# Kernel tuning notes

Hardware: AMD Instinct MI355X
Metric: run time of the kernel (lower is better)

## Reference

```python
import jax, jax.numpy as jnp
import numpy as np

N, IN_DIM = 50000, 1024
E = 100000
NUM_REL = 40
HEADS, OUT_DIM = 4, 200
HID = HEADS * OUT_DIM  # 800
B = 8192
NEG_SLOPE = 0.2


def setup_inputs() -> dict:
    key = jax.random.key(0)
    ks = jax.random.split(key, 12)
    node_emb = jax.random.normal(ks[0], (N, IN_DIM), dtype=jnp.float32)
    # RelGAT learnable params
    W = jax.random.normal(ks[1], (IN_DIM, HID), dtype=jnp.float32) * (1.0 / np.sqrt(IN_DIM))
    bias = jnp.zeros((HID,), dtype=jnp.float32)
    a_src = jax.random.normal(ks[2], (HEADS, OUT_DIM), dtype=jnp.float32) * 0.1
    a_dst = jax.random.normal(ks[3], (HEADS, OUT_DIM), dtype=jnp.float32) * 0.1
    a_rel = jax.random.normal(ks[4], (HEADS, OUT_DIM), dtype=jnp.float32) * 0.1
    rel_feat = jax.random.normal(ks[5], (NUM_REL, HID), dtype=jnp.float32) * 0.1
    # DistMult scorer relation embeddings
    rel_emb = jax.random.normal(ks[6], (NUM_REL, HID), dtype=jnp.float32) * 0.1
    # Graph structure (constants)
    edge_index = jax.random.randint(ks[7], (2, E), 0, N, dtype=jnp.int64)
    edge_type = jax.random.randint(ks[8], (E,), 0, NUM_REL, dtype=jnp.int64)
    # Triple batch
    src_ids = jax.random.randint(ks[9], (B,), 0, N, dtype=jnp.int64)
    rel_ids = jax.random.randint(ks[10], (B,), 0, NUM_REL, dtype=jnp.int64)
    dst_ids = jax.random.randint(ks[11], (B,), 0, N, dtype=jnp.int64)
    return dict(node_emb=node_emb, W=W, bias=bias, a_src=a_src, a_dst=a_dst,
                a_rel=a_rel, rel_feat=rel_feat, rel_emb=rel_emb,
                edge_index=edge_index, edge_type=edge_type,
                src_ids=src_ids, rel_ids=rel_ids, dst_ids=dst_ids)


def _rel_gat(node_emb, W, bias, a_src, a_dst, a_rel, rel_feat, edge_index, edge_type):
    src, dst = edge_index[0], edge_index[1]
    h = (node_emb @ W).reshape(N, HEADS, OUT_DIM)          # [N,H,D]
    hs = h[src]                                            # [E,H,D] gather
    hd = h[dst]                                            # [E,H,D] gather
    r = rel_feat[edge_type].reshape(E, HEADS, OUT_DIM)     # [E,H,D]
    # relation-conditioned attention logits per head
    logits = (jnp.einsum('ehd,hd->eh', hs, a_src)
              + jnp.einsum('ehd,hd->eh', hd, a_dst)
              + jnp.einsum('ehd,hd->eh', r, a_rel))        # [E,H]
    logits = jax.nn.leaky_relu(logits, NEG_SLOPE)
    # segment softmax over incoming edges of each destination node
    seg_max = jax.ops.segment_max(logits, dst, num_segments=N)   # [N,H]
    e = jnp.exp(logits - seg_max[dst])                           # [E,H]
    denom = jax.ops.segment_sum(e, dst, num_segments=N)          # [N,H]
    alpha = e / denom[dst]                                       # [E,H]
    # weighted scatter-aggregate of source messages
    out = jax.ops.segment_sum(alpha[:, :, None] * hs, dst, num_segments=N)  # [N,H,D]
    return out.reshape(N, HID) + bias                            # dropout: eval mode (identity)


def reference(node_emb, W, bias, a_src, a_dst, a_rel, rel_feat, rel_emb,
              edge_index, edge_type, src_ids, rel_ids, dst_ids):
    refined = _rel_gat(node_emb, W, bias, a_src, a_dst, a_rel, rel_feat,
                       edge_index, edge_type)                # [N, HID]
    src_vec = refined[src_ids]                               # [B, HID]
    dst_vec = refined[dst_ids]                               # [B, HID]
    # DistMult: sum(s * r * d)
    scores = jnp.sum(src_vec * rel_emb[rel_ids] * dst_vec, axis=-1)  # [B]
    return scores
```

## Files before the change

kernel.cpp:

```cpp
#include <hip/hip_runtime.h>
#include <hip/hip_bf16.h>
#include <math.h>

#define NN 50000
#define IN_DIM 1024
#define EE 100000
#define NUM_REL 40
#define HEADS 4
#define OUT_D 200
#define HID 800
#define BB 8192
#define SLOT_CAP 16384
#define SRC_CAP 50176
#define WT_COLS 896

typedef __attribute__((ext_vector_type(8))) short short8;
typedef __attribute__((ext_vector_type(4))) float f32x4;

__device__ inline unsigned short f2bf(float f) {
    unsigned int u = __float_as_uint(f);
    u += 0x7FFF + ((u >> 16) & 1);
    return (unsigned short)(u >> 16);
}
__device__ inline float bf2f(unsigned short s) {
    return __uint_as_float(((unsigned int)s) << 16);
}
__device__ inline void gl2lds16(const unsigned short* g, unsigned short* l) {
    __builtin_amdgcn_global_load_lds(
        (const __attribute__((address_space(1))) void*)g,
        (__attribute__((address_space(3))) void*)l, 16, 0, 0);
}

__device__ inline int wave_compact(bool won, int* ctr) {
    unsigned long long m = __ballot(won);
    if (!m) return -1;
    int lane = threadIdx.x & 63;
    int leader = __ffsll((long long)m) - 1;
    int base = 0;
    if (lane == leader) base = atomicAdd(ctr, __popcll(m));
    base = __shfl(base, leader, 64);
    return won ? base + __popcll(m & ((1ull << lane) - 1)) : -1;
}

#define INIT_BLOCKS 196
__global__ __launch_bounds__(256) void k_init_wa(int* slot_of_node, int* xrow_of_node,
                                                 int* deg, int* counters,
                                                 const float* W, const float* a_src,
                                                 const float* a_dst, const float* a_rel,
                                                 const float* rel_feat, float* Wa, float* prel) {
    int b = blockIdx.x;
    if (b < INIT_BLOCKS) {
        int i = b * 256 + threadIdx.x;
        if (i < NN) { slot_of_node[i] = -1; xrow_of_node[i] = -1; }
        if (i < SLOT_CAP) deg[i] = 0;
        if (i < 8) counters[i] = 0;
        return;
    }
    int wid = (b - INIT_BLOCKS) * 4 + (threadIdx.x >> 6);
    int lane = threadIdx.x & 63;
    if (wid >= IN_DIM * 8 + NUM_REL * HEADS) return;
    float acc = 0.f;
    int d = lane * 4;
    if (d < OUT_D) {
        const float* row;
        const float* a;
        if (wid < IN_DIM * 8) {
            int k = wid >> 3, c = wid & 7;
            int h = c & 3;
            row = W + (size_t)k * HID + h * OUT_D;
            a = ((c < 4) ? a_src : a_dst) + h * OUT_D;
        } else {
            int j = wid - IN_DIM * 8;
            int r = j >> 2, h = j & 3;
            row = rel_feat + (size_t)r * HID + h * OUT_D;
            a = a_rel + h * OUT_D;
        }
        float4 wv = *(const float4*)(row + d);
        float4 av = *(const float4*)(a + d);
        acc = wv.x * av.x + wv.y * av.y + wv.z * av.z + wv.w * av.w;
    }
    for (int off = 32; off; off >>= 1) acc += __shfl_down(acc, off, 64);
    if (lane == 0) {
        if (wid < IN_DIM * 8) Wa[wid] = acc;
        else prel[wid - IN_DIM * 8] = acc;
    }
}

__global__ void k_build_slots(const int* src_ids, const int* dst_ids,
                              int* slot_of_node, int* counters, int* scorelist) {
    int i = blockIdx.x * 256 + threadIdx.x;
    bool valid = i < 2 * BB;
    int n = 0;
    bool won = false;
    if (valid) {
        n = (i < BB) ? src_ids[i] : dst_ids[i - BB];
        if (slot_of_node[n] == -1)
            won = (atomicCAS(&slot_of_node[n], -1, -2) == -1);
    }
    int s = wave_compact(won, &counters[0]);
    if (won) {
        slot_of_node[n] = s;
        scorelist[s] = n;
    }
}

__global__ void k_edge0(const int* ei, const int* slot_of_node,
                        int* xrow_of_node, int* counters, int* rows, int* deg) {
    int e = blockIdx.x * 256 + threadIdx.x;
    bool valid = e < EE;
    int slot = -1, sn = 0;
    if (valid) {
        int dn = ei[EE + e];
        slot = slot_of_node[dn];
    }
    bool surv = valid && slot >= 0;
    bool won = false;
    if (surv) {
        sn = ei[e];
        if (xrow_of_node[sn] == -1)
            won = (atomicCAS(&xrow_of_node[sn], -1, -2) == -1);
    }
    int t = wave_compact(won, &counters[1]);
    if (won) {
        rows[t] = sn;
        xrow_of_node[sn] = t;
    }
    if (surv) atomicAdd(&deg[slot], 1);
}

__global__ __launch_bounds__(256) void k_tail_scan_wt(const int* scorelist, int* xrow_of_node,
                                                      int* counters, int* rows,
                                                      const int* deg, int* base, int* cursor,
                                                      const float* W, const float* Wa,
                                                      unsigned short* Wt) {
    int t = threadIdx.x;
    if (blockIdx.x == 0) {
        __shared__ int pref[257];
        int s = 0;
        const int4* dv = (const int4*)(deg + t * (SLOT_CAP / 256));
        for (int i = 0; i < SLOT_CAP / 256 / 4; ++i) {
            int4 v = dv[i];
            s += v.x + v.y + v.z + v.w;
        }
        pref[t + 1] = s;
        if (t == 0) pref[0] = 0;
        __syncthreads();
        if (t == 0)
            for (int i = 1; i <= 256; ++i) pref[i] += pref[i - 1];
        __syncthreads();
        int r = pref[t];
        for (int i = 0; i < SLOT_CAP / 256; ++i) {
            int idx = t * (SLOT_CAP / 256) + i;
            base[idx] = r;
            cursor[idx] = r;
            r += deg[idx];
        }
        return;
    }
    if (blockIdx.x <= 64) {
        int i = (blockIdx.x - 1) * 256 + t;
        bool valid = i < counters[0];
        int n = 0;
        bool won = false;
        if (valid) {
            n = scorelist[i];
            won = (xrow_of_node[n] < 0);
        }
        int tt = wave_compact(won, &counters[3]);
        if (won) {
            int xr = counters[1] + tt;
            xrow_of_node[n] = xr;
            rows[xr] = n;
        }
        return;
    }
    __shared__ float tile[64][65];
    int b = blockIdx.x - 65;
    int k0 = (b & 15) * 64, c0 = (b >> 4) * 64;
    {
        int kk = t >> 2, cc = (t & 3) * 16;
        for (int i = 0; i < 16; ++i) {
            int c = c0 + cc + i;
            float v = 0.f;
            if (c < HID) v = W[(size_t)(k0 + kk) * HID + c];
            else if (c < HID + 8) v = Wa[(size_t)(k0 + kk) * 8 + (c - HID)];
            tile[cc + i][kk] = v;
        }
    }
    __syncthreads();
    {
        int cc = t >> 2, kk = (t & 3) * 16;
        unsigned short o[16];
        for (int i = 0; i < 16; ++i) o[i] = f2bf(tile[cc][kk + i]);
        *(short8*)(Wt + (size_t)(c0 + cc) * IN_DIM + k0 + kk) = *(short8*)o;
        *(short8*)(Wt + (size_t)(c0 + cc) * IN_DIM + k0 + kk + 8) = *(short8*)(o + 8);
    }
}

#define GBM 128
#define GBN 128
#define GBK 64

#define ALOAD(K0) do {                                                  \
    av[0] = *(const float4*)(ax0 + (K0));                               \
    av[1] = *(const float4*)(ax0 + (K0) + 4);                           \
    av[2] = *(const float4*)(ax1 + (K0));                               \
    av[3] = *(const float4*)(ax1 + (K0) + 4);                           \
    av[4] = *(const float4*)(ax0 + (K0) + 32);                          \
    av[5] = *(const float4*)(ax0 + (K0) + 36);                          \
    av[6] = *(const float4*)(ax1 + (K0) + 32);                          \
    av[7] = *(const float4*)(ax1 + (K0) + 36);                          \
} while (0)

#define AWRITE(AS) do {                                                 \
    unsigned short o[8];                                                \
    _Pragma("unroll")                                                   \
    for (int q = 0; q < 4; ++q) {                                       \
        o[0] = f2bf(av[2*q].x); o[1] = f2bf(av[2*q].y);                 \
        o[2] = f2bf(av[2*q].z); o[3] = f2bf(av[2*q].w);                 \
        o[4] = f2bf(av[2*q+1].x); o[5] = f2bf(av[2*q+1].y);             \
        o[6] = f2bf(av[2*q+1].z); o[7] = f2bf(av[2*q+1].w);             \
        *(short8*)&(AS)[(size_t)(q * 256 + t) * 8] = *(short8*)o;       \
    }                                                                   \
} while (0)

#define BSTAGE(BS, K0) do {                                             \
    gl2lds16(bP0 + (K0),      (BS) + (size_t)(0 * 256 + t) * 8);        \
    gl2lds16(bP1 + (K0),      (BS) + (size_t)(1 * 256 + t) * 8);        \
    gl2lds16(bP0 + (K0) + 32, (BS) + (size_t)(2 * 256 + t) * 8);        \
    gl2lds16(bP1 + (K0) + 32, (BS) + (size_t)(3 * 256 + t) * 8);        \
} while (0)

#define COMPUTE(AS, BS) do {                                            \
    _Pragma("unroll")                                                   \
    for (int s = 0; s < 2; ++s) {                                       \
        short8 af[4], bf4[4];                                           \
        _Pragma("unroll")                                               \
        for (int i = 0; i < 4; ++i)                                     \
            af[i] = *(const short8*)&(AS)[(size_t)(s * 512 + (ga + i) * 64 + lane) * 8]; \
        _Pragma("unroll")                                               \
        for (int j = 0; j < 4; ++j)                                     \
            bf4[j] = *(const short8*)&(BS)[(size_t)(s * 512 + (gb + j) * 64 + lane) * 8]; \
        __builtin_amdgcn_s_setprio(1);                                  \
        _Pragma("unroll")                                               \
        for (int i = 0; i < 4; ++i)                                     \
            _Pragma("unroll")                                           \
            for (int j = 0; j < 4; ++j)                                 \
                acc[i][j] = __builtin_amdgcn_mfma_f32_16x16x32_bf16(af[i], bf4[j], acc[i][j], 0, 0, 0); \
        __builtin_amdgcn_s_setprio(0);                                  \
    }                                                                   \
} while (0)

#define WAIT_A  asm volatile("s_waitcnt vmcnt(4)" ::: "memory")
#define PUBLISH asm volatile("s_waitcnt vmcnt(0) lgkmcnt(0)" ::: "memory")
#define BARX    asm volatile("s_barrier" ::: "memory")

__global__ __launch_bounds__(256) void k_hgemm(const float* x, const int* rows,
                                               const unsigned short* Wt,
                                               const int* counters, unsigned short* h_src,
                                               float* sS, float* sD) {
    int nsrc = counters[1];
    int nneed = nsrc + counters[3];
    int lin = blockIdx.x + 7 * blockIdx.y;
    int g = lin / 56, r = lin % 56;
    int rowb = g * 8 + (r & 7);
    int colb = r >> 3;
    int col0 = colb * GBN;
    int row0 = rowb * GBM;
    int rowlim = (col0 == 768) ? nneed : nsrc;
    if (row0 >= rowlim) return;
    __shared__ unsigned short As0[GBM * GBK];
    __shared__ unsigned short As1[GBM * GBK];
    __shared__ unsigned short Bs0[GBN * GBK];
    __shared__ unsigned short Bs1[GBN * GBK];
    int t = threadIdx.x;
    int crow = ((t >> 6) << 4) + (t & 15);
    int coff = ((t >> 4) & 3) << 3;
    int lim = nneed - 1;
    int n0 = rows[min(row0 + crow, lim)];
    int n1 = rows[min(row0 + crow + 64, lim)];
    const float* ax0 = x + (size_t)n0 * IN_DIM + coff;
    const float* ax1 = x + (size_t)n1 * IN_DIM + coff;
    const unsigned short* bP0 = Wt + (size_t)(col0 + crow) * IN_DIM + coff;
    const unsigned short* bP1 = bP0 + (size_t)64 * IN_DIM;
    int w = t >> 6, lane = t & 63;
    int ga = (w >> 1) * 4, gb = (w & 1) * 4;
    int wr = (w >> 1) * 64, wc = (w & 1) * 64;
    int fm = lane & 15, fq = lane >> 4;
    float4 av[8];
    f32x4 acc[4][4] = {};
    ALOAD(0);
    BSTAGE(Bs0, 0);
    WAIT_A;
    AWRITE(As0);
    PUBLISH;
    BARX;
#pragma unroll 1
    for (int kk = 0; kk < 16; kk += 2) {
        ALOAD((kk + 1) * 64);
        BSTAGE(Bs1, (kk + 1) * 64);
        COMPUTE(As0, Bs0);
        BARX;
        WAIT_A;
        AWRITE(As1);
        PUBLISH;
        BARX;
        if (kk < 14) {
            ALOAD((kk + 2) * 64);
            BSTAGE(Bs0, (kk + 2) * 64);
        }
        COMPUTE(As1, Bs1);
        BARX;
        if (kk < 14) {
            WAIT_A;
            AWRITE(As0);
            PUBLISH;
            BARX;
        }
    }
#pragma unroll
    for (int i = 0; i < 4; ++i) {
#pragma unroll
        for (int j = 0; j < 4; ++j) {
            int gcol = col0 + wc + j * 16 + fm;
            if (gcol >= HID + 8) continue;
#pragma unroll
            for (int rr = 0; rr < 4; ++rr) {
                int grow = row0 + wr + i * 16 + fq * 4 + rr;
                float v = acc[i][j][rr];
                if (gcol < HID) {
                    if (grow < nsrc) h_src[(size_t)grow * HID + gcol] = f2bf(v);
                } else if (grow < nneed) {
                    int c = gcol - HID;
                    if (c < 4) sS[grow * 4 + c] = v;
                    else sD[grow * 4 + (c - 4)] = v;
                }
            }
        }
    }
}

__global__ void k_place(const int* ei, const int* etype, const int* slot_of_node,
                        const int* xrow_of_node, int* cursor,
                        const float* sS, const float* sD, const float* prel,
                        float* clogit, int* tlist) {
    int e = blockIdx.x * 256 + threadIdx.x;
    if (e >= EE) return;
    int dn = ei[EE + e];
    int slot = slot_of_node[dn];
    if (slot < 0) return;
    int sn = ei[e];
    int r = etype[e];
    int xs = xrow_of_node[sn];
    int xd = xrow_of_node[dn];
    int pos = atomicAdd(&cursor[slot], 1);
    tlist[pos] = xs;
    float4 lg;
    float* lp = (float*)&lg;
#pragma unroll
    for (int h = 0; h < 4; ++h) {
        float v = sS[xs * 4 + h] + sD[xd * 4 + h] + prel[r * 4 + h];
        lp[h] = v > 0.f ? v : 0.2f * v;
    }
    *(float4*)&clogit[(size_t)pos * 4] = lg;
}

__global__ __launch_bounds__(256) void k_aggregate(const int* counters, const int* base,
                                                   const int* deg, const int* tlist,
                                                   const float* clogit,
                                                   const unsigned short* h_src, const float* bias,
                                                   float* refined) {
    int b = blockIdx.x;
    if (b >= counters[0]) return;
    int beg = base[b], d = deg[b];
    __shared__ float m4[4], den4[4];
    __shared__ float alpha[64][4];
    __shared__ int tsl[64];
    int t = threadIdx.x;
    if (t < 4) {
        float m = -3e38f;
        for (int j = 0; j < d; ++j)
            m = fmaxf(m, clogit[(size_t)(beg + j) * 4 + t]);
        float s = 0.f;
        for (int j = 0; j < d; ++j)
            s += expf(clogit[(size_t)(beg + j) * 4 + t] - m);
        m4[t] = m;
        den4[t] = s;
    }
    __syncthreads();
    int head = t / 50;
    float4 acc = {0.f, 0.f, 0.f, 0.f};
    for (int j0 = 0; j0 < d; j0 += 64) {
        int nc = min(64, d - j0);
        if (t < nc * 4) {
            int j = t >> 2, h = t & 3;
            alpha[j][h] = expf(clogit[(size_t)(beg + j0 + j) * 4 + h] - m4[h]) / den4[h];
            if (h == 0) tsl[j] = tlist[beg + j0 + j];
        }
        __syncthreads();
        if (t < 200) {
            for (int j = 0; j < nc; ++j) {
                float a = alpha[j][head];
                ushort4 hv = *(const ushort4*)(h_src + (size_t)tsl[j] * HID + t * 4);
                acc.x += a * bf2f(hv.x);
                acc.y += a * bf2f(hv.y);
                acc.z += a * bf2f(hv.z);
                acc.w += a * bf2f(hv.w);
            }
        }
        __syncthreads();
    }
    if (t < 200) {
        float4 bv = *(const float4*)(bias + t * 4);
        float4 o = {acc.x + bv.x, acc.y + bv.y, acc.z + bv.z, acc.w + bv.w};
        *(float4*)(refined + (size_t)b * HID + t * 4) = o;
    }
}

__global__ __launch_bounds__(256) void k_score(const int* src_ids, const int* rel_ids,
                                               const int* dst_ids, const int* slot_of_node,
                                               const float* rel_emb, const float* refined,
                                               float* out) {
    int gid = blockIdx.x * 256 + threadIdx.x;
    int b = gid >> 6;
    int lane = threadIdx.x & 63;
    if (b >= BB) return;
    int ss = slot_of_node[src_ids[b]];
    int ds = slot_of_node[dst_ids[b]];
    int r = rel_ids[b];
    const float* sv = refined + (size_t)ss * HID;
    const float* dv = refined + (size_t)ds * HID;
    const float* rv = rel_emb + (size_t)r * HID;
    float acc = 0.f;
    for (int c4 = lane; c4 < 200; c4 += 64) {
        float4 s = *(const float4*)(sv + c4 * 4);
        float4 dq = *(const float4*)(dv + c4 * 4);
        float4 rr = *(const float4*)(rv + c4 * 4);
        acc += s.x * rr.x * dq.x + s.y * rr.y * dq.y + s.z * rr.z * dq.z + s.w * rr.w * dq.w;
    }
    for (int off = 32; off; off >>= 1) acc += __shfl_down(acc, off, 64);
    if (lane == 0) out[b] = acc;
}

extern "C" void kernel_launch(void* const* d_in, const int* in_sizes, int n_in,
                              void* d_out, int out_size, void* d_ws, size_t ws_size,
                              hipStream_t stream) {
    const float* node_emb = (const float*)d_in[0];
    const float* W        = (const float*)d_in[1];
    const float* bias     = (const float*)d_in[2];
    const float* a_src    = (const float*)d_in[3];
    const float* a_dst    = (const float*)d_in[4];
    const float* a_rel    = (const float*)d_in[5];
    const float* rel_feat = (const float*)d_in[6];
    const float* rel_emb  = (const float*)d_in[7];
    const int* edge_index = (const int*)d_in[8];
    const int* edge_type  = (const int*)d_in[9];
    const int* src_ids    = (const int*)d_in[10];
    const int* rel_ids    = (const int*)d_in[11];
    const int* dst_ids    = (const int*)d_in[12];
    float* out = (float*)d_out;

    char* w = (char*)d_ws;
    auto alloc = [&](size_t bytes) -> void* {
        void* p = (void*)w;
        w += (bytes + 255) & ~(size_t)255;
        return p;
    };
    int* slot_of_node = (int*)alloc((size_t)NN * 4);
    int* xrow_of_node = (int*)alloc((size_t)NN * 4);
    int* scorelist    = (int*)alloc((size_t)SLOT_CAP * 4);
    int* rows         = (int*)alloc((size_t)NN * 4);
    int* counters     = (int*)alloc(256);
    int* deg          = (int*)alloc((size_t)SLOT_CAP * 4);
    int* base         = (int*)alloc((size_t)SLOT_CAP * 4);
    int* cursor       = (int*)alloc((size_t)SLOT_CAP * 4);
    int* tlist        = (int*)alloc((size_t)EE * 4);
    float* clogit = (float*)alloc((size_t)EE * 4 * 4);
    float* sS     = (float*)alloc((size_t)SRC_CAP * 4 * 4);
    float* sD     = (float*)alloc((size_t)SRC_CAP * 4 * 4);
    float* Wa     = (float*)alloc((size_t)IN_DIM * 8 * 4);
    float* prel   = (float*)alloc((size_t)NUM_REL * 4 * 4);
    unsigned short* Wt    = (unsigned short*)alloc((size_t)WT_COLS * IN_DIM * 2);
    unsigned short* h_src = (unsigned short*)alloc((size_t)SRC_CAP * HID * 2);
    float* refined = (float*)alloc((size_t)SLOT_CAP * HID * 4);

    int wa_blocks = (IN_DIM * 8 + NUM_REL * HEADS + 3) / 4;
    k_init_wa<<<INIT_BLOCKS + wa_blocks, 256, 0, stream>>>(
        slot_of_node, xrow_of_node, deg, counters,
        W, a_src, a_dst, a_rel, rel_feat, Wa, prel);
    k_build_slots<<<(2 * BB + 255) / 256, 256, 0, stream>>>(src_ids, dst_ids, slot_of_node,
                                                            counters, scorelist);
    k_edge0<<<(EE + 255) / 256, 256, 0, stream>>>(edge_index, slot_of_node,
                                                  xrow_of_node, counters, rows, deg);
    k_tail_scan_wt<<<65 + 224, 256, 0, stream>>>(scorelist, xrow_of_node, counters,
                                                 rows, deg, base, cursor, W, Wa, Wt);
    dim3 ggrid(7, 392);
    k_hgemm<<<ggrid, 256, 0, stream>>>(node_emb, rows, Wt, counters, h_src, sS, sD);
    k_place<<<(EE + 255) / 256, 256, 0, stream>>>(edge_index, edge_type, slot_of_node,
                                                  xrow_of_node, cursor, sS, sD, prel,
                                                  clogit, tlist);
    k_aggregate<<<SLOT_CAP, 256, 0, stream>>>(counters, base, deg, tlist,
                                              clogit, h_src, bias, refined);
    k_score<<<(BB * 64 + 255) / 256, 256, 0, stream>>>(src_ids, rel_ids, dst_ids,
                                                       slot_of_node, rel_emb, refined, out);
}
```

Before: 505.1 us.

## Halve GEMM K-tile, use packed bf16 convert, single barrier per stage

The h-GEMM K tile drops from 64 to 32, so LDS use halves and launch bounds ask for 3 blocks per CU. The scalar round-to-nearest bf16 conversion is replaced with the hardware v_cvt_pk_bf16_f32 instruction. The double-buffered loop is restructured to one wait-plus-barrier per stage instead of two barriers. The aims are higher occupancy and less sync and conversion overhead, at the cost of twice as many loop iterations and less work per barrier.

Result: faster. 492.1 us (-2.6%).

```diff
diff --git a/kernel.cpp b/kernel.cpp
--- a/kernel.cpp
+++ b/kernel.cpp
@@ -29,6 +29,14 @@
     __builtin_amdgcn_global_load_lds(
         (const __attribute__((address_space(1))) void*)g,
         (__attribute__((address_space(3))) void*)l, 16, 0, 0);
+}
+__device__ inline short8 cvt8(float4 u, float4 v) {
+    union { unsigned int w[4]; short8 s; } r;
+    asm("v_cvt_pk_bf16_f32 %0, %1, %2" : "=v"(r.w[0]) : "v"(u.x), "v"(u.y));
+    asm("v_cvt_pk_bf16_f32 %0, %1, %2" : "=v"(r.w[1]) : "v"(u.z), "v"(u.w));
+    asm("v_cvt_pk_bf16_f32 %0, %1, %2" : "=v"(r.w[2]) : "v"(v.x), "v"(v.y));
+    asm("v_cvt_pk_bf16_f32 %0, %1, %2" : "=v"(r.w[3]) : "v"(v.z), "v"(v.w));
+    return r.s;
 }
 
 __device__ inline int wave_compact(bool won, int* ctr) {
@@ -199,66 +207,52 @@
 
 #define GBM 128
 #define GBN 128
-#define GBK 64
-
-#define ALOAD(K0) do {                                                  \
-    av[0] = *(const float4*)(ax0 + (K0));                               \
-    av[1] = *(const float4*)(ax0 + (K0) + 4);                           \
-    av[2] = *(const float4*)(ax1 + (K0));                               \
-    av[3] = *(const float4*)(ax1 + (K0) + 4);                           \
-    av[4] = *(const float4*)(ax0 + (K0) + 32);                          \
-    av[5] = *(const float4*)(ax0 + (K0) + 36);                          \
-    av[6] = *(const float4*)(ax1 + (K0) + 32);                          \
-    av[7] = *(const float4*)(ax1 + (K0) + 36);                          \
+#define GBK 32
+
+#define ALOADR(K) do {                                                  \
+    const float* p0 = ax0 + (size_t)(K) * 32;                           \
+    const float* p1 = ax1 + (size_t)(K) * 32;                           \
+    av0 = *(const float4*)(p0);                                         \
+    av1 = *(const float4*)(p0 + 4);                                     \
+    av2 = *(const float4*)(p1);                                         \
+    av3 = *(const float4*)(p1 + 4);                                     \
 } while (0)
 
 #define AWRITE(AS) do {                                                 \
-    unsigned short o[8];                                                \
+    short8 s0 = cvt8(av0, av1);                                         \
+    short8 s1 = cvt8(av2, av3);                                         \
+    *(short8*)&(AS)[(size_t)t * 8] = s0;                                \
+    *(short8*)&(AS)[(size_t)(256 + t) * 8] = s1;                        \
+} while (0)
+
+#define BSTAGE(BS, K) do {                                              \
+    gl2lds16(bP0 + (size_t)(K) * 32, (BS) + (size_t)t * 8);             \
+    gl2lds16(bP1 + (size_t)(K) * 32, (BS) + (size_t)(256 + t) * 8);     \
+} while (0)
+
+#define COMPUTE(AS, BS) do {                                            \
+    short8 af[4], bf4[4];                                               \
     _Pragma("unroll")                                                   \
-    for (int q = 0; q < 4; ++q) {                                       \
-        o[0] = f2bf(av[2*q].x); o[1] = f2bf(av[2*q].y);                 \
-        o[2] = f2bf(av[2*q].z); o[3] = f2bf(av[2*q].w);                 \
-        o[4] = f2bf(av[2*q+1].x); o[5] = f2bf(av[2*q+1].y);             \
-        o[6] = f2bf(av[2*q+1].z); o[7] = f2bf(av[2*q+1].w);             \
-        *(short8*)&(AS)[(size_t)(q * 256 + t) * 8] = *(short8*)o;       \
-    }                                                                   \
-} while (0)
-
-#define BSTAGE(BS, K0) do {                                             \
-    gl2lds16(bP0 + (K0),      (BS) + (size_t)(0 * 256 + t) * 8);        \
-    gl2lds16(bP1 + (K0),      (BS) + (size_t)(1 * 256 + t) * 8);        \
-    gl2lds16(bP0 + (K0) + 32, (BS) + (size_t)(2 * 256 + t) * 8);        \
-    gl2lds16(bP1 + (K0) + 32, (BS) + (size_t)(3 * 256 + t) * 8);        \
-} while (0)
-
-#define COMPUTE(AS, BS) do {                                            \
+    for (int i = 0; i < 4; ++i)                                         \
+        af[i] = *(const short8*)&(AS)[(size_t)((ga + i) * 64 + lane) * 8]; \
     _Pragma("unroll")                                                   \
-    for (int s = 0; s < 2; ++s) {                                       \
-        short8 af[4], bf4[4];                                           \
-        _Pragma("unroll")                                               \
-        for (int i = 0; i < 4; ++i)                                     \
-            af[i] = *(const short8*)&(AS)[(size_t)(s * 512 + (ga + i) * 64 + lane) * 8]; \
+    for (int j = 0; j < 4; ++j)                                         \
+        bf4[j] = *(const short8*)&(BS)[(size_t)((gb + j) * 64 + lane) * 8]; \
+    __builtin_amdgcn_s_setprio(1);                                      \
+    _Pragma("unroll")                                                   \
+    for (int i = 0; i < 4; ++i)                                         \
         _Pragma("unroll")                                               \
         for (int j = 0; j < 4; ++j)                                     \
-            bf4[j] = *(const short8*)&(BS)[(size_t)(s * 512 + (gb + j) * 64 + lane) * 8]; \
-        __builtin_amdgcn_s_setprio(1);                                  \
-        _Pragma("unroll")                                               \
-        for (int i = 0; i < 4; ++i)                                     \
-            _Pragma("unroll")                                           \
-            for (int j = 0; j < 4; ++j)                                 \
-                acc[i][j] = __builtin_amdgcn_mfma_f32_16x16x32_bf16(af[i], bf4[j], acc[i][j], 0, 0, 0); \
-        __builtin_amdgcn_s_setprio(0);                                  \
-    }                                                                   \
+            acc[i][j] = __builtin_amdgcn_mfma_f32_16x16x32_bf16(af[i], bf4[j], acc[i][j], 0, 0, 0); \
+    __builtin_amdgcn_s_setprio(0);                                      \
 } while (0)
 
-#define WAIT_A  asm volatile("s_waitcnt vmcnt(4)" ::: "memory")
-#define PUBLISH asm volatile("s_waitcnt vmcnt(0) lgkmcnt(0)" ::: "memory")
-#define BARX    asm volatile("s_barrier" ::: "memory")
-
-__global__ __launch_bounds__(256) void k_hgemm(const float* x, const int* rows,
-                                               const unsigned short* Wt,
-                                               const int* counters, unsigned short* h_src,
-                                               float* sS, float* sD) {
+#define GATE asm volatile("s_waitcnt vmcnt(0) lgkmcnt(0)\n\ts_barrier" ::: "memory")
+
+__global__ __launch_bounds__(256, 3) void k_hgemm(const float* x, const int* rows,
+                                                  const unsigned short* Wt,
+                                                  const int* counters, unsigned short* h_src,
+                                                  float* sS, float* sD) {
     int nsrc = counters[1];
     int nneed = nsrc + counters[3];
     int lin = blockIdx.x + 7 * blockIdx.y;
@@ -274,48 +268,40 @@
     __shared__ unsigned short Bs0[GBN * GBK];
     __shared__ unsigned short Bs1[GBN * GBK];
     int t = threadIdx.x;
-    int crow = ((t >> 6) << 4) + (t & 15);
-    int coff = ((t >> 4) & 3) << 3;
+    int r0 = ((t >> 6) << 4) + (t & 15);
+    int ko = ((t >> 4) & 3) << 3;
     int lim = nneed - 1;
-    int n0 = rows[min(row0 + crow, lim)];
-    int n1 = rows[min(row0 + crow + 64, lim)];
-    const float* ax0 = x + (size_t)n0 * IN_DIM + coff;
-    const float* ax1 = x + (size_t)n1 * IN_DIM + coff;
-    const unsigned short* bP0 = Wt + (size_t)(col0 + crow) * IN_DIM + coff;
+    int n0 = rows[min(row0 + r0, lim)];
+    int n1 = rows[min(row0 + r0 + 64, lim)];
+    const float* ax0 = x + (size_t)n0 * IN_DIM + ko;
+    const float* ax1 = x + (size_t)n1 * IN_DIM + ko;
+    const unsigned short* bP0 = Wt + (size_t)(col0 + r0) * IN_DIM + ko;
     const unsigned short* bP1 = bP0 + (size_t)64 * IN_DIM;
     int w = t >> 6, lane = t & 63;
     int ga = (w >> 1) * 4, gb = (w & 1) * 4;
     int wr = (w >> 1) * 64, wc = (w & 1) * 64;
     int fm = lane & 15, fq = lane >> 4;
-    float4 av[8];
+    float4 av0, av1, av2, av3;
     f32x4 acc[4][4] = {};
-    ALOAD(0);
+    ALOADR(0);
     BSTAGE(Bs0, 0);
-    WAIT_A;
     AWRITE(As0);
-    PUBLISH;
-    BARX;
+    GATE;
 #pragma unroll 1
-    for (int kk = 0; kk < 16; kk += 2) {
-        ALOAD((kk + 1) * 64);
-        BSTAGE(Bs1, (kk + 1) * 64);
+    for (int k = 0; k < 32; k += 2) {
+        ALOADR(k + 1);
+        BSTAGE(Bs1, k + 1);
         COMPUTE(As0, Bs0);
-        BARX;
-        WAIT_A;
         AWRITE(As1);
-        PUBLISH;
-        BARX;
-        if (kk < 14) {
-            ALOAD((kk + 2) * 64);
-            BSTAGE(Bs0, (kk + 2) * 64);
+        GATE;
+        if (k < 30) {
+            ALOADR(k + 2);
+            BSTAGE(Bs0, k + 2);
         }
         COMPUTE(As1, Bs1);
-        BARX;
-        if (kk < 14) {
-            WAIT_A;
+        if (k < 30) {
             AWRITE(As0);
-            PUBLISH;
-            BARX;
+            GATE;
         }
     }
 #pragma unroll
```
